# Kernel tuning notes

Measured on AMD Instinct MI355X. Metric: run time of the kernel, lower is better.

## Reference

```python
import jax, jax.numpy as jnp
import numpy as np

CONV_ORDER = 3


def _aggr_norm(L, x):
    # neighborhood_size = row sums of operator; 1/ns with non-finite -> 0
    inv = 1.0 / jnp.sum(L, axis=1)
    inv = jnp.where(jnp.isfinite(inv), inv, 0.0)
    x = inv[:, None] * x
    return jnp.where(jnp.isfinite(x), x, 0.0)


def _chebyshev_conv(L, x, conv_order=CONV_ORDER, aggr_norm=True):
    # Returns [N, C, conv_order]: X[...,k] = norm(L @ X[...,k-1]), X[...,-1 base] = x
    def step(carry, _):
        y = L @ carry
        if aggr_norm:
            y = _aggr_norm(L, y)
        return y, y
    _, X = jax.lax.scan(step, x, None, length=conv_order)  # [K, N, C]
    return jnp.moveaxis(X, 0, -1)  # [N, C, K]


def setup_inputs() -> dict:
    key = jax.random.key(0)
    ks = jax.random.split(key, 13)
    N0, N1, N2, C = 4096, 8192, 4096, 16
    w_scale = 1.414 * np.sqrt(2.0 / (C + C))  # xavier_normal-like
    return {
        "x_0": jax.random.normal(ks[0], (N0, C), jnp.float32),
        "x_1": jax.random.normal(ks[1], (N1, C), jnp.float32),
        "x_2": jax.random.normal(ks[2], (N2, C), jnp.float32),
        "laplacian_0": jax.random.normal(ks[3], (N0, N0), jnp.float32),
        "laplacian_down_1": jax.random.normal(ks[4], (N1, N1), jnp.float32),
        "laplacian_up_1": jax.random.normal(ks[5], (N1, N1), jnp.float32),
        "laplacian_down_2": jax.random.normal(ks[6], (N2, N2), jnp.float32),
        "laplacian_up_2": jax.random.normal(ks[7], (N2, N2), jnp.float32),
        "b1": jax.random.normal(ks[8], (N0, N1), jnp.float32),
        "b2": jax.random.normal(ks[9], (N1, N2), jnp.float32),
        "weight_0": w_scale * jax.random.normal(ks[10], (C, C, 2 + 2 * CONV_ORDER), jnp.float32),
        "weight_1": w_scale * jax.random.normal(ks[11], (C, C, 6 * CONV_ORDER + 3), jnp.float32),
        "weight_2": w_scale * jax.random.normal(ks[12], (C, C, 4 * CONV_ORDER + 2), jnp.float32),
    }


def reference(x_0, x_1, x_2, laplacian_0, laplacian_down_1, laplacian_up_1,
              laplacian_down_2, laplacian_up_2, b1, b2,
              weight_0, weight_1, weight_2):
    # Node-space convolution (the torch forward returns only y_0; the edge/face
    # branches are dead code w.r.t. the returned value and are omitted).
    x_0_lap = _chebyshev_conv(laplacian_0, x_0)                 # [N0, C, K]
    x_0_to_0 = jnp.concatenate([x_0[:, :, None], x_0_lap], axis=2)
    x_1_to_0_upper = b1 @ x_1                                   # [N0, C]
    x_1_to_0_lap = _chebyshev_conv(laplacian_0, x_1_to_0_upper)
    x_1_to_0 = jnp.concatenate([x_1_to_0_upper[:, :, None], x_1_to_0_lap], axis=2)
    x_0_all = jnp.concatenate([x_0_to_0, x_1_to_0], axis=2)     # [N0, C, 2+2K]
    y_0 = jnp.einsum('nik,iok->no', x_0_all, weight_0)
    return y_0
```

## Files before the change

kernel.cpp:

```cpp
#include <hip/hip_runtime.h>
#include <hip/hip_bf16.h>
#include <math.h>

#define N0 4096
#define NM1 8192

template<int NV>
__device__ __forceinline__ void red_scatter(float* v, const int d, const int lane) {
  const bool up = (lane & d) != 0;
  #pragma unroll
  for (int i = 0; i < NV; ++i) {
    float send = up ? v[i] : v[i + NV];
    float recv = __shfl_xor(send, d);
    float keep = up ? v[i + NV] : v[i];
    v[i] = keep + recv;
  }
}

__global__ __launch_bounds__(128)
void b1_matmul_kernel(const float* __restrict__ A,
                      const float* __restrict__ X,
                      float* __restrict__ pP)
{
  __shared__ float4 Bs[2048];
  const int tid  = threadIdx.x;
  const int wv   = tid >> 6;
  const int lane = tid & 63;
  const int q    = lane >> 5;
  const int ml   = lane & 31;
  const int s    = blockIdx.x & 3;
  const int rg   = blockIdx.x >> 2;
  const int row0 = rg * 16 + wv * 8;

  float acc[64];
  #pragma unroll
  for (int i = 0; i < 64; ++i) acc[i] = 0.0f;
  const int j0 = q * 2;

  for (int ch = 0; ch < 4; ++ch) {
    const int mb = s * 2048 + ch * 512;
    __syncthreads();
    #pragma unroll
    for (int k = 0; k < 16; ++k) {
      const int idx = tid + 128 * k;
      const int m = idx >> 2, j = idx & 3;
      Bs[m * 4 + (j ^ ((m >> 1) & 3))] =
          *(const float4*)(X + (size_t)(mb + m) * 16 + j * 4);
    }
    __syncthreads();
    #pragma unroll
    for (int it = 0; it < 4; ++it) {
      float a[8][4];
      #pragma unroll
      for (int r = 0; r < 8; ++r) {
        #pragma unroll
        for (int v = 0; v < 4; ++v)
          a[r][v] = A[(size_t)(row0 + r) * NM1 + mb + it * 128 + ml + 32 * v];
      }
      #pragma unroll
      for (int v = 0; v < 4; ++v) {
        const int mm = it * 128 + ml + 32 * v;
        const int sw = (mm >> 1) & 3;
        const float4 b0 = Bs[mm * 4 + (j0 ^ sw)];
        const float4 b1 = Bs[mm * 4 + ((j0 + 1) ^ sw)];
        #pragma unroll
        for (int r = 0; r < 8; ++r) {
          const float av = a[r][v];
          acc[r*8+0] += av * b0.x;  acc[r*8+1] += av * b0.y;
          acc[r*8+2] += av * b0.z;  acc[r*8+3] += av * b0.w;
          acc[r*8+4] += av * b1.x;  acc[r*8+5] += av * b1.y;
          acc[r*8+6] += av * b1.z;  acc[r*8+7] += av * b1.w;
        }
      }
    }
  }

  red_scatter<32>(acc, 1, lane);
  red_scatter<16>(acc, 2, lane);
  red_scatter<8>(acc, 4, lane);
  red_scatter<4>(acc, 8, lane);
  red_scatter<2>(acc, 16, lane);

  const int r  = ((ml & 1) << 2) | (((ml >> 1) & 1) << 1) | ((ml >> 2) & 1);
  const int cb = ((ml >> 3) & 1) * 4 + ((ml >> 4) & 1) * 2;
  float* dst = pP + (size_t)(s * N0 + row0 + r) * 16 + q * 8 + cb;
  *(float2*)dst = make_float2(acc[0], acc[1]);
}

__global__ void finalize_u_kernel(const float* __restrict__ pP,
                                  float* __restrict__ u) {
  const int idx = blockIdx.x * 256 + threadIdx.x;
  u[idx] = pP[idx] + pP[65536 + idx] + pP[131072 + idx] + pP[196608 + idx];
}

__global__ __launch_bounds__(128)
void cheb_step_kernel(const float* __restrict__ A,
                      const float* __restrict__ cx,
                      const float* __restrict__ cu,
                      float* __restrict__ pX,
                      float* __restrict__ pU,
                      float* __restrict__ pRS)
{
  __shared__ float4 Bs[2048];
  const int tid  = threadIdx.x;
  const int wv   = tid >> 6;
  const int lane = tid & 63;
  const int q    = lane >> 4;
  const int ml   = lane & 15;
  const int s    = blockIdx.x & 3;
  const int rg   = blockIdx.x >> 2;
  const int row0 = rg * 16 + wv * 8;

  float acc[64];
  #pragma unroll
  for (int i = 0; i < 64; ++i) acc[i] = 0.0f;
  float rs[8];
  #pragma unroll
  for (int i = 0; i < 8; ++i) rs[i] = 0.0f;
  const int j0 = q * 2;

  for (int ch = 0; ch < 4; ++ch) {
    const int mb = s * 1024 + ch * 256;
    __syncthreads();
    #pragma unroll
    for (int k = 0; k < 16; ++k) {
      const int idx = tid + 128 * k;
      const int m = idx >> 3, j = idx & 7;
      const float* src = (j < 4) ? (cx + (size_t)(mb + m) * 16 + j * 4)
                                 : (cu + (size_t)(mb + m) * 16 + (j - 4) * 4);
      Bs[m * 8 + (j ^ ((m >> 2) & 7))] = *(const float4*)src;
    }
    __syncthreads();
    #pragma unroll
    for (int it = 0; it < 4; ++it) {
      const int mloc = it * 64 + ml * 4;
      float a[8][4];
      #pragma unroll
      for (int r = 0; r < 8; ++r) {
        const float4 t = *(const float4*)(A + (size_t)(row0 + r) * N0 + mb + mloc);
        a[r][0] = t.x; a[r][1] = t.y; a[r][2] = t.z; a[r][3] = t.w;
      }
      #pragma unroll
      for (int v = 0; v < 4; ++v) {
        const int mm = mloc + v;
        const int sw = (mm >> 2) & 7;
        const float4 b0 = Bs[mm * 8 + (j0 ^ sw)];
        const float4 b1 = Bs[mm * 8 + ((j0 + 1) ^ sw)];
        #pragma unroll
        for (int r = 0; r < 8; ++r) {
          const float av = a[r][v];
          acc[r*8+0] += av * b0.x;  acc[r*8+1] += av * b0.y;
          acc[r*8+2] += av * b0.z;  acc[r*8+3] += av * b0.w;
          acc[r*8+4] += av * b1.x;  acc[r*8+5] += av * b1.y;
          acc[r*8+6] += av * b1.z;  acc[r*8+7] += av * b1.w;
          rs[r] += av;
        }
      }
    }
  }

  red_scatter<32>(acc, 1, lane);
  red_scatter<16>(acc, 2, lane);
  red_scatter<8>(acc, 4, lane);
  red_scatter<4>(acc, 8, lane);

  red_scatter<4>(rs, 1, lane);
  red_scatter<2>(rs, 2, lane);
  red_scatter<1>(rs, 4, lane);
  const float rsum = rs[0] + __shfl_xor(rs[0], 8);

  const int r  = ((ml & 1) << 2) | (((ml >> 1) & 1) << 1) | ((ml >> 2) & 1);
  const int cb = ((ml >> 3) & 1) * 4;
  float* base = (q >> 1) ? pU : pX;
  float* dst = base + (size_t)(s * N0 + row0 + r) * 16 + (q & 1) * 8 + cb;
  *(float4*)dst = make_float4(acc[0], acc[1], acc[2], acc[3]);

  if (q == 0 && ml < 8) pRS[s * N0 + row0 + r] = rsum;
}

__global__ void normalize_kernel(const float* __restrict__ pX,
                                 const float* __restrict__ pU,
                                 const float* __restrict__ pRS,
                                 float* __restrict__ ox,
                                 float* __restrict__ ou) {
  const int idx = blockIdx.x * 256 + threadIdx.x;
  const int row = idx >> 4;
  float rsv = pRS[row] + pRS[N0 + row] + pRS[2 * N0 + row] + pRS[3 * N0 + row];
  float inv = 1.0f / rsv;
  if (!isfinite(inv)) inv = 0.0f;
  float xv = (pX[idx] + pX[65536 + idx] + pX[131072 + idx] + pX[196608 + idx]) * inv;
  float uv = (pU[idx] + pU[65536 + idx] + pU[131072 + idx] + pU[196608 + idx]) * inv;
  ox[idx] = isfinite(xv) ? xv : 0.0f;
  ou[idx] = isfinite(uv) ? uv : 0.0f;
}

__global__ void einsum_kernel(const float* __restrict__ x0,
                              const float* __restrict__ xl1,
                              const float* __restrict__ xl2,
                              const float* __restrict__ xl3,
                              const float* __restrict__ u,
                              const float* __restrict__ ul1,
                              const float* __restrict__ ul2,
                              const float* __restrict__ ul3,
                              const float* __restrict__ W,
                              float* __restrict__ y) {
  __shared__ float Wl[2048];
  __shared__ float xs[16 * 128];
  const int t = threadIdx.x;
  const int row0 = blockIdx.x * 16;
  #pragma unroll
  for (int k = 0; k < 8; ++k) Wl[t + 256 * k] = W[t + 256 * k];
  const int r = t >> 4;
  const int i = t & 15;
  const int g = (row0 + r) * 16 + i;
  xs[r * 128 + 0 * 16 + i] = x0[g];
  xs[r * 128 + 1 * 16 + i] = xl1[g];
  xs[r * 128 + 2 * 16 + i] = xl2[g];
  xs[r * 128 + 3 * 16 + i] = xl3[g];
  xs[r * 128 + 4 * 16 + i] = u[g];
  xs[r * 128 + 5 * 16 + i] = ul1[g];
  xs[r * 128 + 6 * 16 + i] = ul2[g];
  xs[r * 128 + 7 * 16 + i] = ul3[g];
  __syncthreads();
  const int o = t & 15;
  float acc = 0.0f;
  #pragma unroll
  for (int ii = 0; ii < 16; ++ii) {
    #pragma unroll
    for (int k = 0; k < 8; ++k)
      acc += xs[r * 128 + k * 16 + ii] * Wl[(ii * 16 + o) * 8 + k];
  }
  y[(row0 + r) * 16 + o] = acc;
}

extern "C" void kernel_launch(void* const* d_in, const int* in_sizes, int n_in,
                              void* d_out, int out_size, void* d_ws, size_t ws_size,
                              hipStream_t stream) {
  const float* x0 = (const float*)d_in[0];
  const float* x1 = (const float*)d_in[1];
  const float* L0 = (const float*)d_in[3];
  const float* B1 = (const float*)d_in[8];
  const float* W0 = (const float*)d_in[10];

  float* ws  = (float*)d_ws;
  float* u   = ws;
  float* xl1 = ws + 65536;
  float* xl2 = ws + 131072;
  float* xl3 = ws + 196608;
  float* ul1 = ws + 262144;
  float* ul2 = ws + 327680;
  float* ul3 = ws + 393216;
  float* pX  = ws + 458752;
  float* pU  = ws + 720896;
  float* pRS = ws + 983040;

  b1_matmul_kernel<<<1024, 128, 0, stream>>>(B1, x1, pX);
  finalize_u_kernel<<<256, 256, 0, stream>>>(pX, u);

  cheb_step_kernel<<<1024, 128, 0, stream>>>(L0, x0, u, pX, pU, pRS);
  normalize_kernel<<<256, 256, 0, stream>>>(pX, pU, pRS, xl1, ul1);
  cheb_step_kernel<<<1024, 128, 0, stream>>>(L0, xl1, ul1, pX, pU, pRS);
  normalize_kernel<<<256, 256, 0, stream>>>(pX, pU, pRS, xl2, ul2);
  cheb_step_kernel<<<1024, 128, 0, stream>>>(L0, xl2, ul2, pX, pU, pRS);
  normalize_kernel<<<256, 256, 0, stream>>>(pX, pU, pRS, xl3, ul3);

  einsum_kernel<<<256, 256, 0, stream>>>(x0, xl1, xl2, xl3, u, ul1, ul2, ul3,
                                         W0, (float*)d_out);
}
```

Measured before the change: 163.3 us.

## Use 256-thread blocks with fewer rows per wave, cache inverse row sums, fuse final normalize

The matmul kernels now run 4 waves per block, each handling 4 rows instead of 8. This halves the accumulator registers and raises occupancy, and B1 loads become float4. The row-sum inverse is computed once in the first Chebyshev step, and the later steps skip the row-sum work through a template flag. The last normalize is folded into the einsum kernel, which drops one launch and one intermediate buffer round-trip, at the cost of more partial-sum reads inside the einsum.

New measurement: 136.5 us. 16.4% less time.

```diff
diff --git a/kernel.cpp b/kernel.cpp
--- a/kernel.cpp
+++ b/kernel.cpp
@@ -17,7 +17,7 @@
   }
 }
 
-__global__ __launch_bounds__(128)
+__global__ __launch_bounds__(256)
 void b1_matmul_kernel(const float* __restrict__ A,
                       const float* __restrict__ X,
                       float* __restrict__ pP)
@@ -30,61 +30,61 @@
   const int ml   = lane & 31;
   const int s    = blockIdx.x & 3;
   const int rg   = blockIdx.x >> 2;
-  const int row0 = rg * 16 + wv * 8;
-
-  float acc[64];
-  #pragma unroll
-  for (int i = 0; i < 64; ++i) acc[i] = 0.0f;
+  const int row0 = rg * 16 + wv * 4;
+
+  float acc[32];
+  #pragma unroll
+  for (int i = 0; i < 32; ++i) acc[i] = 0.0f;
   const int j0 = q * 2;
+  const int jj = tid & 3;
+  const int mt = tid >> 2;
 
   for (int ch = 0; ch < 4; ++ch) {
     const int mb = s * 2048 + ch * 512;
     __syncthreads();
     #pragma unroll
-    for (int k = 0; k < 16; ++k) {
-      const int idx = tid + 128 * k;
-      const int m = idx >> 2, j = idx & 3;
-      Bs[m * 4 + (j ^ ((m >> 1) & 3))] =
-          *(const float4*)(X + (size_t)(mb + m) * 16 + j * 4);
+    for (int k = 0; k < 8; ++k) {
+      const int m = mt + 64 * k;
+      Bs[(m * 4 + jj) ^ ((m >> 2) & 7)] =
+          *(const float4*)(X + (size_t)(mb + m) * 16 + jj * 4);
     }
     __syncthreads();
     #pragma unroll
     for (int it = 0; it < 4; ++it) {
-      float a[8][4];
-      #pragma unroll
-      for (int r = 0; r < 8; ++r) {
+      const int mloc = it * 128 + ml * 4;
+      float a[4][4];
+      #pragma unroll
+      for (int r = 0; r < 4; ++r) {
+        const float4 t4 = *(const float4*)(A + (size_t)(row0 + r) * NM1 + mb + mloc);
+        a[r][0] = t4.x; a[r][1] = t4.y; a[r][2] = t4.z; a[r][3] = t4.w;
+      }
+      #pragma unroll
+      for (int v = 0; v < 4; ++v) {
+        const int mm = mloc + v;
+        const int h = (mm >> 2) & 7;
+        const float4 b0  = Bs[(mm * 4 + j0) ^ h];
+        const float4 b1v = Bs[(mm * 4 + j0 + 1) ^ h];
         #pragma unroll
-        for (int v = 0; v < 4; ++v)
-          a[r][v] = A[(size_t)(row0 + r) * NM1 + mb + it * 128 + ml + 32 * v];
-      }
-      #pragma unroll
-      for (int v = 0; v < 4; ++v) {
-        const int mm = it * 128 + ml + 32 * v;
-        const int sw = (mm >> 1) & 3;
-        const float4 b0 = Bs[mm * 4 + (j0 ^ sw)];
-        const float4 b1 = Bs[mm * 4 + ((j0 + 1) ^ sw)];
-        #pragma unroll
-        for (int r = 0; r < 8; ++r) {
+        for (int r = 0; r < 4; ++r) {
           const float av = a[r][v];
-          acc[r*8+0] += av * b0.x;  acc[r*8+1] += av * b0.y;
-          acc[r*8+2] += av * b0.z;  acc[r*8+3] += av * b0.w;
-          acc[r*8+4] += av * b1.x;  acc[r*8+5] += av * b1.y;
-          acc[r*8+6] += av * b1.z;  acc[r*8+7] += av * b1.w;
+          acc[r*8+0] += av * b0.x;   acc[r*8+1] += av * b0.y;
+          acc[r*8+2] += av * b0.z;   acc[r*8+3] += av * b0.w;
+          acc[r*8+4] += av * b1v.x;  acc[r*8+5] += av * b1v.y;
+          acc[r*8+6] += av * b1v.z;  acc[r*8+7] += av * b1v.w;
         }
       }
     }
   }
 
-  red_scatter<32>(acc, 1, lane);
-  red_scatter<16>(acc, 2, lane);
-  red_scatter<8>(acc, 4, lane);
-  red_scatter<4>(acc, 8, lane);
-  red_scatter<2>(acc, 16, lane);
-
-  const int r  = ((ml & 1) << 2) | (((ml >> 1) & 1) << 1) | ((ml >> 2) & 1);
-  const int cb = ((ml >> 3) & 1) * 4 + ((ml >> 4) & 1) * 2;
-  float* dst = pP + (size_t)(s * N0 + row0 + r) * 16 + q * 8 + cb;
-  *(float2*)dst = make_float2(acc[0], acc[1]);
+  red_scatter<16>(acc, 1, lane);
+  red_scatter<8>(acc, 2, lane);
+  red_scatter<4>(acc, 4, lane);
+  red_scatter<2>(acc, 8, lane);
+  red_scatter<1>(acc, 16, lane);
+
+  const int r = 2 * (ml & 1) + ((ml >> 1) & 1);
+  const int c = 4 * ((ml >> 2) & 1) + 2 * ((ml >> 3) & 1) + ((ml >> 4) & 1);
+  pP[(size_t)(s * N0 + row0 + r) * 16 + q * 8 + c] = acc[0];
 }
 
 __global__ void finalize_u_kernel(const float* __restrict__ pP,
@@ -93,7 +93,8 @@
   u[idx] = pP[idx] + pP[65536 + idx] + pP[131072 + idx] + pP[196608 + idx];
 }
 
-__global__ __launch_bounds__(128)
+template<bool RS>
+__global__ __launch_bounds__(256)
 void cheb_step_kernel(const float* __restrict__ A,
                       const float* __restrict__ cx,
                       const float* __restrict__ cu,
@@ -109,87 +110,104 @@
   const int ml   = lane & 15;
   const int s    = blockIdx.x & 3;
   const int rg   = blockIdx.x >> 2;
-  const int row0 = rg * 16 + wv * 8;
-
-  float acc[64];
-  #pragma unroll
-  for (int i = 0; i < 64; ++i) acc[i] = 0.0f;
-  float rs[8];
-  #pragma unroll
-  for (int i = 0; i < 8; ++i) rs[i] = 0.0f;
+  const int row0 = rg * 16 + wv * 4;
+
+  float acc[32];
+  #pragma unroll
+  for (int i = 0; i < 32; ++i) acc[i] = 0.0f;
+  float rs[4] = {0.0f, 0.0f, 0.0f, 0.0f};
   const int j0 = q * 2;
+
+  const int jj   = tid & 7;
+  const int mt   = tid >> 3;
+  const float* sbase = (jj < 4) ? cx : cu;
+  const int joff = (jj & 3) * 4;
 
   for (int ch = 0; ch < 4; ++ch) {
     const int mb = s * 1024 + ch * 256;
     __syncthreads();
     #pragma unroll
-    for (int k = 0; k < 16; ++k) {
-      const int idx = tid + 128 * k;
-      const int m = idx >> 3, j = idx & 7;
-      const float* src = (j < 4) ? (cx + (size_t)(mb + m) * 16 + j * 4)
-                                 : (cu + (size_t)(mb + m) * 16 + (j - 4) * 4);
-      Bs[m * 8 + (j ^ ((m >> 2) & 7))] = *(const float4*)src;
+    for (int k = 0; k < 8; ++k) {
+      const int m = mt + 32 * k;
+      Bs[(m * 8 + jj) ^ ((m >> 2) & 7)] =
+          *(const float4*)(sbase + (size_t)(mb + m) * 16 + joff);
     }
     __syncthreads();
     #pragma unroll
     for (int it = 0; it < 4; ++it) {
       const int mloc = it * 64 + ml * 4;
-      float a[8][4];
-      #pragma unroll
-      for (int r = 0; r < 8; ++r) {
-        const float4 t = *(const float4*)(A + (size_t)(row0 + r) * N0 + mb + mloc);
-        a[r][0] = t.x; a[r][1] = t.y; a[r][2] = t.z; a[r][3] = t.w;
+      float a[4][4];
+      #pragma unroll
+      for (int r = 0; r < 4; ++r) {
+        const float4 t4 = *(const float4*)(A + (size_t)(row0 + r) * N0 + mb + mloc);
+        a[r][0] = t4.x; a[r][1] = t4.y; a[r][2] = t4.z; a[r][3] = t4.w;
       }
       #pragma unroll
       for (int v = 0; v < 4; ++v) {
         const int mm = mloc + v;
-        const int sw = (mm >> 2) & 7;
-        const float4 b0 = Bs[mm * 8 + (j0 ^ sw)];
-        const float4 b1 = Bs[mm * 8 + ((j0 + 1) ^ sw)];
+        const int h = (mm >> 2) & 7;
+        const float4 b0  = Bs[(mm * 8 + j0) ^ h];
+        const float4 b1v = Bs[(mm * 8 + j0 + 1) ^ h];
         #pragma unroll
-        for (int r = 0; r < 8; ++r) {
+        for (int r = 0; r < 4; ++r) {
           const float av = a[r][v];
-          acc[r*8+0] += av * b0.x;  acc[r*8+1] += av * b0.y;
-          acc[r*8+2] += av * b0.z;  acc[r*8+3] += av * b0.w;
-          acc[r*8+4] += av * b1.x;  acc[r*8+5] += av * b1.y;
-          acc[r*8+6] += av * b1.z;  acc[r*8+7] += av * b1.w;
-          rs[r] += av;
+          acc[r*8+0] += av * b0.x;   acc[r*8+1] += av * b0.y;
+          acc[r*8+2] += av * b0.z;   acc[r*8+3] += av * b0.w;
+          acc[r*8+4] += av * b1v.x;  acc[r*8+5] += av * b1v.y;
+          acc[r*8+6] += av * b1v.z;  acc[r*8+7] += av * b1v.w;
+          if constexpr (RS) rs[r] += av;
         }
       }
     }
   }
 
-  red_scatter<32>(acc, 1, lane);
-  red_scatter<16>(acc, 2, lane);
-  red_scatter<8>(acc, 4, lane);
-  red_scatter<4>(acc, 8, lane);
-
-  red_scatter<4>(rs, 1, lane);
-  red_scatter<2>(rs, 2, lane);
-  red_scatter<1>(rs, 4, lane);
-  const float rsum = rs[0] + __shfl_xor(rs[0], 8);
-
-  const int r  = ((ml & 1) << 2) | (((ml >> 1) & 1) << 1) | ((ml >> 2) & 1);
-  const int cb = ((ml >> 3) & 1) * 4;
+  red_scatter<16>(acc, 1, lane);
+  red_scatter<8>(acc, 2, lane);
+  red_scatter<4>(acc, 4, lane);
+  red_scatter<2>(acc, 8, lane);
+
+  const int r  = 2 * (ml & 1) + ((ml >> 1) & 1);
+  const int cL = 4 * ((ml >> 2) & 1) + 2 * ((ml >> 3) & 1);
   float* base = (q >> 1) ? pU : pX;
-  float* dst = base + (size_t)(s * N0 + row0 + r) * 16 + (q & 1) * 8 + cb;
-  *(float4*)dst = make_float4(acc[0], acc[1], acc[2], acc[3]);
-
-  if (q == 0 && ml < 8) pRS[s * N0 + row0 + r] = rsum;
-}
-
-__global__ void normalize_kernel(const float* __restrict__ pX,
-                                 const float* __restrict__ pU,
-                                 const float* __restrict__ pRS,
-                                 float* __restrict__ ox,
-                                 float* __restrict__ ou) {
+  float* dst = base + (size_t)(s * N0 + row0 + r) * 16 + (q & 1) * 8 + cL;
+  *(float2*)dst = make_float2(acc[0], acc[1]);
+
+  if constexpr (RS) {
+    red_scatter<2>(rs, 1, lane);
+    red_scatter<1>(rs, 2, lane);
+    float rsum = rs[0] + __shfl_xor(rs[0], 4);
+    rsum += __shfl_xor(rsum, 8);
+    if (q == 0 && ml < 4) pRS[s * N0 + row0 + r] = rsum;
+  }
+}
+
+__global__ void norm1_kernel(const float* __restrict__ pX,
+                             const float* __restrict__ pU,
+                             const float* __restrict__ pRS,
+                             float* __restrict__ inv,
+                             float* __restrict__ ox,
+                             float* __restrict__ ou) {
   const int idx = blockIdx.x * 256 + threadIdx.x;
   const int row = idx >> 4;
   float rsv = pRS[row] + pRS[N0 + row] + pRS[2 * N0 + row] + pRS[3 * N0 + row];
-  float inv = 1.0f / rsv;
-  if (!isfinite(inv)) inv = 0.0f;
-  float xv = (pX[idx] + pX[65536 + idx] + pX[131072 + idx] + pX[196608 + idx]) * inv;
-  float uv = (pU[idx] + pU[65536 + idx] + pU[131072 + idx] + pU[196608 + idx]) * inv;
+  float iv = 1.0f / rsv;
+  if (!isfinite(iv)) iv = 0.0f;
+  if ((idx & 15) == 0) inv[row] = iv;
+  float xv = (pX[idx] + pX[65536 + idx] + pX[131072 + idx] + pX[196608 + idx]) * iv;
+  float uv = (pU[idx] + pU[65536 + idx] + pU[131072 + idx] + pU[196608 + idx]) * iv;
+  ox[idx] = isfinite(xv) ? xv : 0.0f;
+  ou[idx] = isfinite(uv) ? uv : 0.0f;
+}
+
+__global__ void norm23_kernel(const float* __restrict__ pX,
+                              const float* __restrict__ pU,
+                              const float* __restrict__ inv,
+                              float* __restrict__ ox,
+                              float* __restrict__ ou) {
+  const int idx = blockIdx.x * 256 + threadIdx.x;
+  const float iv = inv[idx >> 4];
+  float xv = (pX[idx] + pX[65536 + idx] + pX[131072 + idx] + pX[196608 + idx]) * iv;
+  float uv = (pU[idx] + pU[65536 + idx] + pU[131072 + idx] + pU[196608 + idx]) * iv;
   ox[idx] = isfinite(xv) ? xv : 0.0f;
   ou[idx] = isfinite(uv) ? uv : 0.0f;
 }
@@ -197,11 +215,12 @@
 __global__ void einsum_kernel(const float* __restrict__ x0,
                               const float* __restrict__ xl1,
                               const float* __restrict__ xl2,
-                              const float* __restrict__ xl3,
                               const float* __restrict__ u,
                               const float* __restrict__ ul1,
                               const float* __restrict__ ul2,
-                              const float* __restrict__ ul3,
+                              const float* __restrict__ pX,
+                              const float* __restrict__ pU,
+                              const float* __restrict__ inv,
                               const float* __restrict__ W,
                               float* __restrict__ y) {
   __shared__ float Wl[2048];
@@ -213,14 +232,19 @@
   const int r = t >> 4;
   const int i = t & 15;
   const int g = (row0 + r) * 16 + i;
+  const float iv = inv[row0 + r];
+  float x3 = (pX[g] + pX[65536 + g] + pX[131072 + g] + pX[196608 + g]) * iv;
+  float u3 = (pU[g] + pU[65536 + g] + pU[131072 + g] + pU[196608 + g]) * iv;
+  if (!isfinite(x3)) x3 = 0.0f;
+  if (!isfinite(u3)) u3 = 0.0f;
   xs[r * 128 + 0 * 16 + i] = x0[g];
   xs[r * 128 + 1 * 16 + i] = xl1[g];
   xs[r * 128 + 2 * 16 + i] = xl2[g];
-  xs[r * 128 + 3 * 16 + i] = xl3[g];
+  xs[r * 128 + 3 * 16 + i] = x3;
   xs[r * 128 + 4 * 16 + i] = u[g];
   xs[r * 128 + 5 * 16 + i] = ul1[g];
   xs[r * 128 + 6 * 16 + i] = ul2[g];
-  xs[r * 128 + 7 * 16 + i] = ul3[g];
+  xs[r * 128 + 7 * 16 + i] = u3;
   __syncthreads();
   const int o = t & 15;
   float acc = 0.0f;
@@ -246,24 +270,22 @@
   float* u   = ws;
   float* xl1 = ws + 65536;
   float* xl2 = ws + 131072;
-  float* xl3 = ws + 196608;
-  float* ul1 = ws + 262144;
-  float* ul2 = ws + 327680;
-  float* ul3 = ws + 393216;
-  float* pX  = ws + 458752;
-  float* pU  = ws + 720896;
-  float* pRS = ws + 983040;
-
-  b1_matmul_kernel<<<1024, 128, 0, stream>>>(B1, x1, pX);
+  float* ul1 = ws + 196608;
+  float* ul2 = ws + 262144;
+  float* inv = ws + 327680;
+  float* pX  = ws + 331776;
+  float* pU  = ws + 593920;
+  float* pRS = ws + 856064;
+
+  b1_matmul_kernel<<<1024, 256, 0, stream>>>(B1, x1, pX);
   finalize_u_kernel<<<256, 256, 0, stream>>>(pX, u);
 
-  cheb_step_kernel<<<1024, 128, 0, stream>>>(L0, x0, u, pX, pU, pRS);
-  normalize_kernel<<<256, 256, 0, stream>>>(pX, pU, pRS, xl1, ul1);
-  cheb_step_kernel<<<1024, 128, 0, stream>>>(L0, xl1, ul1, pX, pU, pRS);
-  normalize_kernel<<<256, 256, 0, stream>>>(pX, pU, pRS, xl2, ul2);
-  cheb_step_kernel<<<1024, 128, 0, stream>>>(L0, xl2, ul2, pX, pU, pRS);
-  normalize_kernel<<<256, 256, 0, stream>>>(pX, pU, pRS, xl3, ul3);
-
-  einsum_kernel<<<256, 256, 0, stream>>>(x0, xl1, xl2, xl3, u, ul1, ul2, ul3,
-                                         W0, (float*)d_out);
-}
+  cheb_step_kernel<true><<<1024, 256, 0, stream>>>(L0, x0, u, pX, pU, pRS);
+  norm1_kernel<<<256, 256, 0, stream>>>(pX, pU, pRS, inv, xl1, ul1);
+  cheb_step_kernel<false><<<1024, 256, 0, stream>>>(L0, xl1, ul1, pX, pU, pRS);
+  norm23_kernel<<<256, 256, 0, stream>>>(pX, pU, inv, xl2, ul2);
+  cheb_step_kernel<false><<<1024, 256, 0, stream>>>(L0, xl2, ul2, pX, pU, pRS);
+
+  einsum_kernel<<<256, 256, 0, stream>>>(x0, xl1, xl2, u, ul1, ul2,
+                                         pX, pU, inv, W0, (float*)d_out);
+}
```
